# Kernel tuning notes

Hardware: AMD Instinct MI355X
Metric: run time of the kernel (lower is better)

The kernel has to match this reference:

```python
import jax, jax.numpy as jnp
import numpy as np
from jax.scipy.special import xlogy

NUM_TTA = 64
FILTER_VIEWS = 0.1
KEPT_VIEWS = int(FILTER_VIEWS * NUM_TTA)  # 6
EPS = 1e-8


def setup_inputs() -> dict:
    key = jax.random.key(0)
    k1, k2 = jax.random.split(key)
    x = jax.random.normal(k1, (16384, 4096), dtype=jnp.float32)
    W = jax.random.normal(k2, (4096, 1000), dtype=jnp.float32) * 0.02
    b = jnp.zeros((1000,), dtype=jnp.float32)
    return {"x": x, "W": W, "b": b}


def reference(x, W, b):
    # inner model: linear + softmax -> per-view class probabilities
    probs = jax.nn.softmax(x @ W + b, axis=-1)            # (B*V, C)
    C = probs.shape[-1]
    B = probs.shape[0] // NUM_TTA
    probs = probs.reshape(B, NUM_TTA, C)                  # (b v c)

    # entr(p).sum(-1) == -sum p*log p (entr(0)=0 handled by xlogy)
    entropies = -xlogy(probs, probs).sum(-1)              # (B, V)
    conf_idx = jnp.argsort(entropies, axis=-1)            # most confident first
    votes = jnp.argmax(probs, axis=-1)                    # (B, V)
    sorted_votes = jnp.take_along_axis(votes, conf_idx, axis=1)  # (B, V)

    # initial majority vote over the KEPT_VIEWS most confident views
    counts = jax.nn.one_hot(sorted_votes[:, :KEPT_VIEWS], C, dtype=jnp.float32).sum(1)  # (B, C)

    rows = jnp.arange(B)

    # sequential tie-breaking: while there is a tie at the max, add the next
    # most confident view's vote; at most NUM_TTA - KEPT_VIEWS extra views.
    def body(i, counts):
        maximum = counts.max(axis=-1, keepdims=True)       # (B, 1)
        tied = (counts == maximum).sum(axis=-1) > 1        # (B,)
        cls = sorted_votes[:, KEPT_VIEWS + i]              # (B,)
        return counts.at[rows, cls].add(tied.astype(counts.dtype))

    counts = jax.lax.fori_loop(0, NUM_TTA - KEPT_VIEWS, body, counts)

    predictions = counts / NUM_TTA
    return jnp.log(predictions + EPS)
```

## Files before the change

kernel.cpp:

```cpp
#include <hip/hip_runtime.h>
#include <cstdint>
#include <cstddef>
#include <math.h>

#define M_ROWS 16384
#define N_COLS 1000
#define N_PAD  1024
#define K_DIM  4096
#define NUM_TTA 64
#define KEPT 6
#define BATCH 256
#define NKT (K_DIM / 32)

typedef __attribute__((ext_vector_type(8))) short short8;
typedef __attribute__((ext_vector_type(4))) float v4f;

#define GL_LDS16(g, l)                                                        \
    __builtin_amdgcn_global_load_lds(                                         \
        (const __attribute__((address_space(1))) unsigned int*)(g),           \
        (__attribute__((address_space(3))) unsigned int*)(l), 16, 0, 0)

__device__ __forceinline__ void split2(float x, unsigned short& h, unsigned short& l) {
    const __bf16 hb = (__bf16)x;
    const float hf  = (float)hb;
    const __bf16 lb = (__bf16)(x - hf);
    h = __builtin_bit_cast(unsigned short, hb);
    l = __builtin_bit_cast(unsigned short, lb);
}

__device__ __forceinline__ void split8(const float4& a, const float4& b,
                                       short8& hv, short8& lv) {
    unsigned short h, l;
    split2(a.x, h, l); hv[0] = (short)h; lv[0] = (short)l;
    split2(a.y, h, l); hv[1] = (short)h; lv[1] = (short)l;
    split2(a.z, h, l); hv[2] = (short)h; lv[2] = (short)l;
    split2(a.w, h, l); hv[3] = (short)h; lv[3] = (short)l;
    split2(b.x, h, l); hv[4] = (short)h; lv[4] = (short)l;
    split2(b.y, h, l); hv[5] = (short)h; lv[5] = (short)l;
    split2(b.z, h, l); hv[6] = (short)h; lv[6] = (short)l;
    split2(b.w, h, l); hv[7] = (short)h; lv[7] = (short)l;
}

__device__ __forceinline__ double exp_neg(double d) {
    if (d < -700.0) return 0.0;
    const double kd = rint(d * 1.4426950408889634074);
    double r = fma(-kd, 6.93147180369123816490e-01, d);
    r = fma(-kd, 1.90821492927058770002e-10, r);
    double p = 2.08767569878680989792e-09;
    p = fma(p, r, 2.50521083854417187751e-08);
    p = fma(p, r, 2.75573192239858906526e-07);
    p = fma(p, r, 2.75573192239858925110e-06);
    p = fma(p, r, 2.48015873015873015873e-05);
    p = fma(p, r, 1.98412698412698412526e-04);
    p = fma(p, r, 1.38888888888888894069e-03);
    p = fma(p, r, 8.33333333333333321769e-03);
    p = fma(p, r, 4.16666666666666643537e-02);
    p = fma(p, r, 1.66666666666666657415e-01);
    p = fma(p, r, 5.0e-01);
    p = fma(p, r, 1.0);
    p = fma(p, r, 1.0);
    const long long k = (long long)kd;
    return p * __longlong_as_double((1023LL + k) << 52);
}

__global__ __launch_bounds__(1024)
void split_w(const float* __restrict__ W, unsigned short* __restrict__ Wh,
             unsigned short* __restrict__ Wl)
{
    __shared__ float tile[32][33];
    const int k0 = blockIdx.x * 32, n0 = blockIdx.y * 32;
    const int tx = threadIdx.x, ty = threadIdx.y;
    const int n = n0 + tx, k = k0 + ty;
    tile[ty][tx] = (n < N_COLS) ? W[(size_t)k * N_COLS + n] : 0.f;
    __syncthreads();
    const float w = tile[tx][ty];
    unsigned short h, l;
    split2(w, h, l);
    const size_t o = (size_t)(n0 + ty) * K_DIM + k0 + tx;
    Wh[o] = h; Wl[o] = l;
}

__global__ __launch_bounds__(512, 2)
void gemm_mfma(const float* __restrict__ X,
               const unsigned short* __restrict__ Bh_, const unsigned short* __restrict__ Bl_,
               const float* __restrict__ bias, double* __restrict__ part,
               int m_tiles)
{
    __shared__ __attribute__((aligned(16))) char smem[2 * 4 * 16384];

    const int t    = threadIdx.x;
    const int lane = t & 63;
    const int wave = t >> 6;
    const int wr   = wave >> 2;
    const int wc   = wave & 3;
    const int ml   = lane & 15;
    const int kh   = lane >> 4;

    const int bid  = blockIdx.x;
    const int xcd  = bid & 7;
    const int slot = bid >> 3;
    const int mt   = xcd * (m_tiles >> 3) + (slot >> 2);
    const int nt   = slot & 3;
    const int m0 = mt * 256, n0 = nt * 256;

    const int    schunk = (t & 3) ^ ((t >> 3) & 3);
    const size_t ro     = (size_t)(t >> 2) * (K_DIM * 2) + (size_t)schunk * 16;
    const char* gBh = (const char*)Bh_ + (size_t)n0 * (K_DIM * 2) + ro;
    const char* gBl = (const char*)Bl_ + (size_t)n0 * (K_DIM * 2) + ro;
    char* ldst = smem + t * 16;
    const size_t RSTEP = (size_t)128 * K_DIM * 2;

    const int ar    = t >> 1;
    const int ahalf = t & 1;
    const float* gA = X + (size_t)(m0 + ar) * K_DIM + ahalf * 16;
    const int sig = (ar >> 1) & 3;
    const int s0  = (ahalf * 2) ^ sig;
    const int s1  = (ahalf * 2 + 1) ^ sig;
    const int aw0 = ar * 64 + (s0 << 4);
    const int aw1 = ar * 64 + (s1 << 4);

    const int swz = ((kh ^ (ml >> 1)) & 3) << 4;
    const int lbA = wr * 8192 + ml * 64 + swz;
    const int lbB = wc * 4096 + ml * 64 + swz;

    v4f acc[8][4];
#pragma unroll
    for (int i = 0; i < 8; ++i)
#pragma unroll
        for (int j = 0; j < 4; ++j) acc[i][j] = (v4f){0.f, 0.f, 0.f, 0.f};

#define FRAG(P) (*(const short8*)(smem + (P)))
#define SB __builtin_amdgcn_sched_barrier(0)

    short8 ah[4], al[4], bh[4], bl[4];

    {
        const float4 fa = *(const float4*)(gA);
        const float4 fb = *(const float4*)(gA + 4);
        const float4 fc = *(const float4*)(gA + 8);
        const float4 fd = *(const float4*)(gA + 12);
        GL_LDS16(gBh,         ldst + 32768);
        GL_LDS16(gBh + RSTEP, ldst + 40960);
        GL_LDS16(gBl,         ldst + 49152);
        GL_LDS16(gBl + RSTEP, ldst + 57344);
        short8 hv, lv;
        split8(fa, fb, hv, lv);
        *(short8*)(smem + aw0) = hv;
        *(short8*)(smem + 16384 + aw0) = lv;
        split8(fc, fd, hv, lv);
        *(short8*)(smem + aw1) = hv;
        *(short8*)(smem + 16384 + aw1) = lv;
    }
    __syncthreads();

#define RD_B(NF) do {                                                         \
    bh[NF] = FRAG(B0 + 32768 + (NF) * 1024 + lbB);                            \
    bl[NF] = FRAG(B0 + 49152 + (NF) * 1024 + lbB);                            \
} while (0)
#define RD_A(MF, HO) do {                                                     \
    ah[MF] = FRAG(B0 + (HO) +         (MF) * 1024 + lbA);                     \
    al[MF] = FRAG(B0 + (HO) + 16384 + (MF) * 1024 + lbA);                     \
} while (0)
#define MCLN(NF) do {                                                         \
    __builtin_amdgcn_s_setprio(1);                                            \
    _Pragma("unroll")                                                         \
    for (int mf = 0; mf < 4; ++mf)                                            \
        acc[mf][NF] = __builtin_amdgcn_mfma_f32_16x16x32_bf16(ah[mf], bl[NF], acc[mf][NF], 0, 0, 0); \
    _Pragma("unroll")                                                         \
    for (int mf = 0; mf < 4; ++mf)                                            \
        acc[mf][NF] = __builtin_amdgcn_mfma_f32_16x16x32_bf16(al[mf], bh[NF], acc[mf][NF], 0, 0, 0); \
    _Pragma("unroll")                                                         \
    for (int mf = 0; mf < 4; ++mf)                                            \
        acc[mf][NF] = __builtin_amdgcn_mfma_f32_16x16x32_bf16(ah[mf], bh[NF], acc[mf][NF], 0, 0, 0); \
    __builtin_amdgcn_s_setprio(0);                                            \
} while (0)
#define MCLM(MF) do {                                                         \
    __builtin_amdgcn_s_setprio(1);                                            \
    _Pragma("unroll")                                                         \
    for (int nf = 0; nf < 4; ++nf)                                            \
        acc[4 + (MF)][nf] = __builtin_amdgcn_mfma_f32_16x16x32_bf16(ah[MF], bl[nf], acc[4 + (MF)][nf], 0, 0, 0); \
    _Pragma("unroll")                                                         \
    for (int nf = 0; nf < 4; ++nf)                                            \
        acc[4 + (MF)][nf] = __builtin_amdgcn_mfma_f32_16x16x32_bf16(al[MF], bh[nf], acc[4 + (MF)][nf], 0, 0, 0); \
    _Pragma("unroll")                                                         \
    for (int nf = 0; nf < 4; ++nf)                                            \
        acc[4 + (MF)][nf] = __builtin_amdgcn_mfma_f32_16x16x32_bf16(ah[MF], bh[nf], acc[4 + (MF)][nf], 0, 0, 0); \
    __builtin_amdgcn_s_setprio(0);                                            \
} while (0)

#define TILE_BODY(KT, RB) do {                                                \
    const int B0 = (RB) * 65536;                                              \
    const int B1 = ((RB) ^ 1) * 65536;                                        \
    asm volatile("s_waitcnt vmcnt(0) lgkmcnt(0)" ::: "memory");               \
    __builtin_amdgcn_s_barrier();                                             \
    SB;                                                                       \
    const bool pf = (KT) + 1 < NKT;                                           \
    float4 fa, fb;                                                            \
    if (pf) {                                                                 \
        const float* ga_ = gA + ((KT) + 1) * 32;                              \
        fa = *(const float4*)(ga_);                                           \
        fb = *(const float4*)(ga_ + 4);                                       \
        const int kb_ = ((KT) + 1) * 64;                                      \
        GL_LDS16(gBh + kb_,         ldst + B1 + 32768);                       \
        GL_LDS16(gBh + RSTEP + kb_, ldst + B1 + 40960);                       \
        GL_LDS16(gBl + kb_,         ldst + B1 + 49152);                       \
        GL_LDS16(gBl + RSTEP + kb_, ldst + B1 + 57344);                       \
    }                                                                         \
    RD_B(0);                                                                  \
    RD_A(0, 0); RD_A(1, 0); RD_A(2, 0); RD_A(3, 0);                           \
    RD_B(1);                                                                  \
    SB;                                                                       \
    MCLN(0); SB;                                                              \
    RD_B(2); SB;                                                              \
    MCLN(1); SB;                                                              \
    RD_B(3); SB;                                                              \
    MCLN(2); SB;                                                              \
    MCLN(3); SB;                                                              \
    RD_A(0, 4096); RD_A(1, 4096); SB;                                         \
    MCLM(0); SB;                                                              \
    if (pf) {                                                                 \
        short8 hv, lv;                                                        \
        split8(fa, fb, hv, lv);                                               \
        *(short8*)(smem + B1 + aw0) = hv;                                     \
        *(short8*)(smem + B1 + 16384 + aw0) = lv;                             \
        const float* ga_ = gA + ((KT) + 1) * 32 + 8;                          \
        fa = *(const float4*)(ga_);                                           \
        fb = *(const float4*)(ga_ + 4);                                       \
    }                                                                         \
    SB;                                                                       \
    RD_A(2, 4096); SB;                                                        \
    MCLM(1); SB;                                                              \
    RD_A(3, 4096); SB;                                                        \
    MCLM(2); SB;                                                              \
    if (pf) {                                                                 \
        short8 hv, lv;                                                        \
        split8(fa, fb, hv, lv);                                               \
        *(short8*)(smem + B1 + aw1) = hv;                                     \
        *(short8*)(smem + B1 + 16384 + aw1) = lv;                             \
    }                                                                         \
    SB;                                                                       \
    MCLM(3);                                                                  \
} while (0)

#pragma unroll 1
    for (int kt = 0; kt < NKT; kt += 2) {
        TILE_BODY(kt, 0);
        TILE_BODY(kt + 1, 1);
    }

    const int chunk = nt * 4 + wc;
    const int colbase = n0 + wc * 64;
    float bcol[4]; bool bval[4];
#pragma unroll
    for (int ni = 0; ni < 4; ++ni) {
        const int col = colbase + ni * 16 + ml;
        bval[ni] = (col < N_COLS);
        bcol[ni] = bval[ni] ? bias[col] : 0.f;
    }
#pragma unroll
    for (int mi = 0; mi < 8; ++mi) {
        const int rbase = m0 + wr * 128 + (mi >> 2) * 64 + (mi & 3) * 16 + kh * 4;
#pragma unroll
        for (int r = 0; r < 4; ++r) {
            float x[4];
            float bv = -3.0e38f; int bi = 0;
#pragma unroll
            for (int ni = 0; ni < 4; ++ni) {
                x[ni] = acc[mi][ni][r] + bcol[ni];
                const int col = colbase + ni * 16 + ml;
                if (bval[ni] && x[ni] > bv) { bv = x[ni]; bi = col; }
            }
#pragma unroll
            for (int s = 8; s > 0; s >>= 1) {
                const float ov = __shfl_xor(bv, s);
                const int   oi = __shfl_xor(bi, s);
                if (ov > bv || (ov == bv && oi < bi)) { bv = ov; bi = oi; }
            }
            float S = 0.f, T = 0.f;
#pragma unroll
            for (int ni = 0; ni < 4; ++ni) {
                if (bval[ni]) {
                    const float d = x[ni] - bv;
                    const float e = __expf(d);
                    S += e;
                    T = fmaf(e, d, T);
                }
            }
#pragma unroll
            for (int s = 8; s > 0; s >>= 1) {
                S += __shfl_xor(S, s);
                T += __shfl_xor(T, s);
            }
            if (ml == 0) {
                double* pp = part + ((size_t)(rbase + r) * 16 + chunk) * 4;
                pp[0] = (double)S; pp[1] = (double)T;
                pp[2] = (double)bv; pp[3] = (double)bi;
            }
        }
    }
#undef TILE_BODY
#undef MCLM
#undef MCLN
#undef RD_A
#undef RD_B
#undef SB
#undef FRAG
}

__global__ __launch_bounds__(64)
void vote_kernel(const double* __restrict__ part, float* __restrict__ out)
{
    __shared__ double e[NUM_TTA];
    __shared__ int    sv[NUM_TTA];
    __shared__ float  counts[N_COLS];

    const int b = blockIdx.x;
    const int t = threadIdx.x;
    const int row = b * NUM_TTA + t;

    const double* pp = part + (size_t)row * 64;
    float m = -3.0e38f; int amax = 0;
#pragma unroll
    for (int c = 0; c < 16; ++c) {
        const float pm = (float)pp[c * 4 + 2];
        const int   pa = (int)pp[c * 4 + 3];
        if (pm > m) { m = pm; amax = pa; }
    }
    double S = 0.0, T = 0.0;
#pragma unroll
    for (int c = 0; c < 16; ++c) {
        const double dm = (double)((float)pp[c * 4 + 2]) - (double)m;
        const double f  = exp_neg(dm);
        S += pp[c * 4 + 0] * f;
        T += (pp[c * 4 + 1] + dm * pp[c * 4 + 0]) * f;
    }
    e[t] = log(S) - T / S;
    const int myv = amax;
    for (int c = t; c < N_COLS; c += NUM_TTA) counts[c] = 0.f;
    __syncthreads();

    const double et = e[t];
    int rank = 0;
#pragma unroll
    for (int i = 0; i < NUM_TTA; ++i) {
        const double ei = e[i];
        rank += (ei < et) || (ei == et && i < t);
    }
    sv[rank] = myv;
    __syncthreads();

    if (t == 0) {
        for (int j = 0; j < KEPT; ++j) counts[sv[j]] += 1.f;
        float Mv = 0.f; int Tc = 0;
        for (int j = 0; j < KEPT; ++j) {
            const int c = sv[j];
            bool dup = false;
            for (int q = 0; q < j; ++q) dup = dup || (sv[q] == c);
            if (dup) continue;
            const float cv = counts[c];
            if (cv > Mv) { Mv = cv; Tc = 1; }
            else if (cv == Mv) { Tc += 1; }
        }
        for (int i = 0; i < NUM_TTA - KEPT; ++i) {
            if (Tc <= 1) break;
            const int c = sv[KEPT + i];
            const float oldc = counts[c];
            counts[c] = oldc + 1.f;
            if (oldc == Mv)            { Mv += 1.f; Tc = 1; }
            else if (oldc + 1.f == Mv) { Tc += 1; }
        }
    }
    __syncthreads();

    const size_t o0 = (size_t)b * N_COLS;
    for (int c = t; c < N_COLS; c += NUM_TTA)
        out[o0 + c] = logf(counts[c] * (1.f / 64.f) + 1e-8f);
}

extern "C" void kernel_launch(void* const* d_in, const int* in_sizes, int n_in,
                              void* d_out, int out_size, void* d_ws, size_t ws_size,
                              hipStream_t stream) {
    const float* x    = (const float*)d_in[0];
    const float* Wm   = (const float*)d_in[1];
    const float* bias = (const float*)d_in[2];
    float* out = (float*)d_out;

    char* p = (char*)d_ws;
    double* part = (double*)p;                     p += (size_t)M_ROWS * 16 * 4 * 8;
    unsigned short* Wh = (unsigned short*)p;       p += (size_t)N_PAD * K_DIM * 2;
    unsigned short* Wl = (unsigned short*)p;       p += (size_t)N_PAD * K_DIM * 2;

    split_w<<<dim3(K_DIM / 32, N_PAD / 32), dim3(32, 32), 0, stream>>>(Wm, Wh, Wl);

    const int m_tiles = M_ROWS / 256;
    gemm_mfma<<<4 * m_tiles, 512, 0, stream>>>(
        x, Wh, Wl, bias, part, m_tiles);
    vote_kernel<<<BATCH, NUM_TTA, 0, stream>>>(part, out);
}
```

Baseline: 634.5 us.

## Software-pipeline the last two MFMA clusters across the K-tile barrier

Restructures the GEMM main loop so the final two low-half MFMA clusters (MCLM 2,3) of each K tile run after the next tile's barrier. Their A fragments are read at the end of the previous tile and held in registers. The intent is to overlap that tail compute with the next tile's barrier wait and LDS reads, removing the stall at each tile boundary. It adds a peeled prologue and epilogue, and keeping extra fragments live raises register pressure.

```diff
diff --git a/kernel.cpp b/kernel.cpp
--- a/kernel.cpp
+++ b/kernel.cpp
@@ -188,7 +188,7 @@
     __builtin_amdgcn_s_setprio(0);                                            \
 } while (0)
 
-#define TILE_BODY(KT, RB) do {                                                \
+#define TILE_X(KT, RB, PREV) do {                                             \
     const int B0 = (RB) * 65536;                                              \
     const int B1 = ((RB) ^ 1) * 65536;                                        \
     asm volatile("s_waitcnt vmcnt(0) lgkmcnt(0)" ::: "memory");               \
@@ -196,7 +196,7 @@
     SB;                                                                       \
     const bool pf = (KT) + 1 < NKT;                                           \
     float4 fa, fb;                                                            \
-    if (pf) {                                                                 \
+    if (pf) {             \
         const float* ga_ = gA + ((KT) + 1) * 32;                              \
         fa = *(const float4*)(ga_);                                           \
         fb = *(const float4*)(ga_ + 4);                                       \
@@ -206,19 +206,20 @@
         GL_LDS16(gBl + kb_,         ldst + B1 + 49152);                       \
         GL_LDS16(gBl + RSTEP + kb_, ldst + B1 + 57344);                       \
     }                                                                         \
-    RD_B(0);                                                                  \
-    RD_A(0, 0); RD_A(1, 0); RD_A(2, 0); RD_A(3, 0);                           \
-    RD_B(1);                                                                  \
+                      \
+    RD_A(0, 0); RD_A(1, 0);                                                   \
+    SB;                                                                       \
+    if (PREV) {     \
+        MCLM(2); MCLM(3);                                                     \
+    }                                                                         \
+    SB;                                                                       \
+                  \
+    RD_A(2, 0); RD_A(3, 0);                                                   \
+    RD_B(0); RD_B(1); RD_B(2); RD_B(3);                                       \
     SB;                                                                       \
     MCLN(0); SB;                                                              \
-    RD_B(2); SB;                                                              \
     MCLN(1); SB;                                                              \
-    RD_B(3); SB;                                                              \
-    MCLN(2); SB;                                                              \
-    MCLN(3); SB;                                                              \
-    RD_A(0, 4096); RD_A(1, 4096); SB;                                         \
-    MCLM(0); SB;                                                              \
-    if (pf) {                                                                 \
+    if (pf) {           \
         short8 hv, lv;                                                        \
         split8(fa, fb, hv, lv);                                               \
         *(short8*)(smem + B1 + aw0) = hv;                                     \
@@ -228,25 +229,33 @@
         fb = *(const float4*)(ga_ + 4);                                       \
     }                                                                         \
     SB;                                                                       \
-    RD_A(2, 4096); SB;                                                        \
-    MCLM(1); SB;                                                              \
-    RD_A(3, 4096); SB;                                                        \
-    MCLM(2); SB;                                                              \
-    if (pf) {                                                                 \
+    MCLN(2); SB;                                                              \
+    MCLN(3); SB;                                                              \
+    RD_A(0, 4096); RD_A(1, 4096); SB;                                         \
+    MCLM(0); SB;                                                              \
+    if (pf) {                                 \
         short8 hv, lv;                                                        \
         split8(fa, fb, hv, lv);                                               \
         *(short8*)(smem + B1 + aw1) = hv;                                     \
         *(short8*)(smem + B1 + 16384 + aw1) = lv;                             \
     }                                                                         \
     SB;                                                                       \
-    MCLM(3);                                                                  \
+    MCLM(1); SB;                                                              \
+           \
+       \
+    RD_A(2, 4096); RD_A(3, 4096);                                             \
 } while (0)
 
+    TILE_X(0, 0, 0);
 #pragma unroll 1
-    for (int kt = 0; kt < NKT; kt += 2) {
-        TILE_BODY(kt, 0);
-        TILE_BODY(kt + 1, 1);
-    }
+    for (int kt = 1; kt + 1 < NKT; kt += 2) {
+        TILE_X(kt, 1, 1);
+        TILE_X(kt + 1, 0, 1);
+    }
+    TILE_X(NKT - 1, 1, 1);
+    asm volatile("s_waitcnt lgkmcnt(0)");
+    SB;
+    MCLM(2); MCLM(3);
 
     const int chunk = nt * 4 + wc;
     const int colbase = n0 + wc * 64;
@@ -298,7 +307,7 @@
             }
         }
     }
-#undef TILE_BODY
+#undef TILE_X
 #undef MCLM
 #undef MCLN
 #undef RD_A
```

Measured after the change: 734.3 us. +15.7%, slower.
